# Kernel optimization log

Hardware: AMD Instinct MI355X
Metric: run time of the kernel (lower is better)

The kernel has to match this reference:

```python
import jax, jax.numpy as jnp
import numpy as np

D_MODEL = 1024
NUM_HEADS = 16
D_IN = 1024

def setup_inputs() -> dict:
    key = jax.random.key(0)
    ks = jax.random.split(key, 5)
    scale = 1.0 / np.sqrt(D_IN)
    return {
        "in_features": jax.random.normal(ks[0], (4, 2048, D_IN), dtype=jnp.float32),
        "q_weight": jax.random.normal(ks[1], (D_MODEL, D_IN), dtype=jnp.float32) * scale,
        "k_weight": jax.random.normal(ks[2], (D_MODEL, D_IN), dtype=jnp.float32) * scale,
        "v_weight": jax.random.normal(ks[3], (D_MODEL, D_IN), dtype=jnp.float32) * scale,
        "o_weight": jax.random.normal(ks[4], (D_MODEL, D_MODEL), dtype=jnp.float32) * scale,
    }

def reference(in_features, q_weight, k_weight, v_weight, o_weight):
    batch, seq_len, _ = in_features.shape
    d_head = D_MODEL // NUM_HEADS
    # QKV projections (Linear with no bias: x @ W^T)
    q = jnp.einsum('bsi,di->bsd', in_features, q_weight)
    k = jnp.einsum('bsi,di->bsd', in_features, k_weight)
    v = jnp.einsum('bsi,di->bsd', in_features, v_weight)
    # split heads -> [b, h, s, d_head]
    q = q.reshape(batch, seq_len, NUM_HEADS, d_head).transpose(0, 2, 1, 3)
    k = k.reshape(batch, seq_len, NUM_HEADS, d_head).transpose(0, 2, 1, 3)
    v = v.reshape(batch, seq_len, NUM_HEADS, d_head).transpose(0, 2, 1, 3)
    # scaled dot-product attention (scale by per-head dim, as in SelfAttention)
    scores = jnp.einsum('bhqd,bhkd->bhqk', q, k) / jnp.sqrt(jnp.float32(d_head))
    probs = jax.nn.softmax(scores, axis=-1)
    ctx = jnp.einsum('bhqk,bhkd->bhqd', probs, v)
    # merge heads -> [b, s, d_model]
    ctx = ctx.transpose(0, 2, 1, 3).reshape(batch, seq_len, D_MODEL)
    # output projection
    return jnp.einsum('bsd,md->bsm', ctx, o_weight)
```

## Files before the change

### kernel.cpp

```cpp
#include <hip/hip_runtime.h>

typedef _Float16 half8 __attribute__((ext_vector_type(8)));
typedef _Float16 half4v __attribute__((ext_vector_type(4)));
typedef float f32x4 __attribute__((ext_vector_type(4)));
typedef float f32x16 __attribute__((ext_vector_type(16)));

__device__ __forceinline__ void gload_lds16(const _Float16* g, _Float16* l) {
    __builtin_amdgcn_global_load_lds(
        (const __attribute__((address_space(1))) void*)g,
        (__attribute__((address_space(3))) void*)l,
        16, 0, 0);
}

__global__ void cvt_f32_f16(const float* __restrict__ src, _Float16* __restrict__ dst, int n4) {
    int i = blockIdx.x * blockDim.x + threadIdx.x;
    if (i >= n4) return;
    f32x4 v = ((const f32x4*)src)[i];
    half4v h;
    h[0] = (_Float16)v[0]; h[1] = (_Float16)v[1];
    h[2] = (_Float16)v[2]; h[3] = (_Float16)v[3];
    ((half4v*)dst)[i] = h;
}

__global__ void cvt4_f32_f16(const float* __restrict__ s0, const float* __restrict__ s1,
                             const float* __restrict__ s2, const float* __restrict__ s3,
                             _Float16* __restrict__ dst) {
    int i = blockIdx.x * blockDim.x + threadIdx.x;
    int wsel = blockIdx.y;
    const float* src = (wsel == 0) ? s0 : (wsel == 1) ? s1 : (wsel == 2) ? s2 : s3;
    f32x4 v = ((const f32x4*)src)[i];
    half4v h;
    h[0] = (_Float16)v[0]; h[1] = (_Float16)v[1];
    h[2] = (_Float16)v[2]; h[3] = (_Float16)v[3];
    ((half4v*)(dst + (size_t)wsel * 1048576))[i] = h;
}

template<int MODE>
__global__ void gemm_nt(const _Float16* __restrict__ A,
                        const _Float16* __restrict__ Wbase,
                        void* __restrict__ outbase)
{
    constexpr int K = 1024;
    __shared__ _Float16 As[2][128 * 32];
    __shared__ _Float16 Bs[2][128 * 32];

    const int tid  = threadIdx.x;
    const int lane = tid & 63;
    const int w    = tid >> 6;
    const int wr   = w >> 1, wc = w & 1;
    const int lr   = lane & 15, lg = lane >> 4;
    const int brow = blockIdx.x * 128;
    const int bcol = blockIdx.y * 128;

    const _Float16* Bw = Wbase + (MODE == 0 ? (size_t)blockIdx.z * (1024u * 1024u) : 0);

    const int srow = w * 16 + (lane >> 2);
    const int scol = (lane & 3) * 8;
    const _Float16* Ag = A  + (size_t)(brow + srow) * K + scol;
    const _Float16* Bg = Bw + (size_t)(bcol + srow) * K + scol;

    auto stage = [&](int buf, int kt) {
        const _Float16* a0 = Ag + kt * 32;
        const _Float16* b0 = Bg + kt * 32;
        gload_lds16(a0,           &As[buf][w * 512]);
        gload_lds16(a0 + 64 * K,  &As[buf][w * 512 + 2048]);
        gload_lds16(b0,           &Bs[buf][w * 512]);
        gload_lds16(b0 + 64 * K,  &Bs[buf][w * 512 + 2048]);
    };

    f32x4 acc[4][4] = {};
    stage(0, 0);
    __syncthreads();

    for (int kt = 0; kt < K / 32; ++kt) {
        const int cur = kt & 1;
        if (kt + 1 < K / 32) stage(cur ^ 1, kt + 1);
        half8 af[4], bf[4];
#pragma unroll
        for (int mi = 0; mi < 4; ++mi)
            af[mi] = *(const half8*)&As[cur][(wr * 64 + mi * 16 + lr) * 32 + lg * 8];
#pragma unroll
        for (int ni = 0; ni < 4; ++ni)
            bf[ni] = *(const half8*)&Bs[cur][(wc * 64 + ni * 16 + lr) * 32 + lg * 8];
#pragma unroll
        for (int mi = 0; mi < 4; ++mi)
#pragma unroll
            for (int ni = 0; ni < 4; ++ni)
                acc[mi][ni] = __builtin_amdgcn_mfma_f32_16x16x32_f16(af[mi], bf[ni], acc[mi][ni], 0, 0, 0);
        __syncthreads();
    }

    if (MODE == 0) {
        _Float16* outp = (_Float16*)outbase + (size_t)blockIdx.z * (8192u * 1024u);
        if (blockIdx.z == 2) {
            _Float16* Ts = &As[0][0];
#pragma unroll
            for (int p = 0; p < 2; ++p) {
                if (wc == p) {
#pragma unroll
                    for (int mi = 0; mi < 4; ++mi)
#pragma unroll
                        for (int ni = 0; ni < 4; ++ni) {
                            int drow = ni * 16 + lr;
                            int s0   = wr * 64 + mi * 16 + lg * 4;
                            half4v o;
#pragma unroll
                            for (int r = 0; r < 4; ++r) o[r] = (_Float16)acc[mi][ni][r];
                            int byteoff = drow * 256 + s0 * 2;
                            byteoff ^= (drow & 7) << 4;
                            *(half4v*)((char*)Ts + byteoff) = o;
                        }
                }
                __syncthreads();
                {
                    int row   = tid >> 2;
                    int cbase = (tid & 3) * 4;
                    int gd = bcol + p * 64 + row;
                    int h = gd >> 6, dd = gd & 63;
                    int b = brow >> 11, sseq = brow & 2047;
                    _Float16* gout = outp + (((size_t)b * 16 + h) * 64 + dd) * 2048 + sseq;
#pragma unroll
                    for (int j = 0; j < 4; ++j) {
                        int c  = cbase + j;
                        int lc = c ^ (row & 7);
                        half8 v = *(const half8*)&Ts[row * 128 + lc * 8];
                        *(half8*)&gout[c * 8] = v;
                    }
                }
                __syncthreads();
            }
        } else {
            const float scale = (blockIdx.z == 0) ? 0.18033688f : 1.0f;
#pragma unroll
            for (int mi = 0; mi < 4; ++mi)
#pragma unroll
                for (int ni = 0; ni < 4; ++ni)
#pragma unroll
                    for (int r = 0; r < 4; ++r) {
                        int row = brow + wr * 64 + mi * 16 + lg * 4 + r;
                        int col = bcol + wc * 64 + ni * 16 + lr;
                        int b = row >> 11, s = row & 2047;
                        int h = col >> 6,  d = col & 63;
                        outp[(((size_t)b * 16 + h) * 2048 + s) * 64 + d] =
                            (_Float16)(acc[mi][ni][r] * scale);
                    }
        }
    } else {
        float* outp = (float*)outbase;
#pragma unroll
        for (int mi = 0; mi < 4; ++mi)
#pragma unroll
            for (int ni = 0; ni < 4; ++ni)
#pragma unroll
                for (int r = 0; r < 4; ++r) {
                    int row = brow + wr * 64 + mi * 16 + lg * 4 + r;
                    int col = bcol + wc * 64 + ni * 16 + lr;
                    outp[(size_t)row * 1024 + col] = acc[mi][ni][r];
                }
    }
}

__global__ __launch_bounds__(256, 4)
void attn_kernel(const _Float16* __restrict__ Q,
                 const _Float16* __restrict__ Kx,
                 const _Float16* __restrict__ Vt,
                 _Float16* __restrict__ Ctx)
{
    __shared__ _Float16 Ks[2][64 * 72];
    __shared__ _Float16 Vs[2][64 * 72];

    const int tid = threadIdx.x, lane = tid & 63, w = tid >> 6;
    const int l31 = lane & 31, hi = lane >> 5;
    const int bh = blockIdx.y, qblk = blockIdx.x;

    const _Float16* Qp  = Q  + ((size_t)bh * 2048 + qblk * 128) * 64;
    const _Float16* Kp  = Kx + (size_t)bh * 2048 * 64;
    const _Float16* Vtp = Vt + (size_t)bh * 64 * 2048;

    half8 qf[4];
#pragma unroll
    for (int ks = 0; ks < 4; ++ks)
        qf[ks] = *(const half8*)(Qp + (size_t)(w * 32 + l31) * 64 + ks * 16 + hi * 8);

    half8 ones;
#pragma unroll
    for (int e = 0; e < 8; ++e) ones[e] = (_Float16)1.0f;

    const int srow = tid >> 3;
    const int scol = (tid & 7) * 8;
    const _Float16* Kg0 = Kp  + (size_t)srow * 64   + scol;
    const _Float16* Vg0 = Vtp + (size_t)srow * 2048 + scol;
    const int ldso = srow * 72 + scol;

    f32x16 cacc[2] = {};
    f32x16 lsum = {};
    float m = -1e30f;

    half8 kr0, kr1, vr0, vr1;
    kr0 = *(const half8*)(Kg0);
    kr1 = *(const half8*)(Kg0 + 32 * 64);
    vr0 = *(const half8*)(Vg0);
    vr1 = *(const half8*)(Vg0 + 32 * 2048);
    *(half8*)&Ks[0][ldso]           = kr0;
    *(half8*)&Ks[0][ldso + 32 * 72] = kr1;
    *(half8*)&Vs[0][ldso]           = vr0;
    *(half8*)&Vs[0][ldso + 32 * 72] = vr1;
    __syncthreads();

    for (int t = 0; t < 32; ++t) {
        const int cur = t & 1;
        if (t < 31) {
            kr0 = *(const half8*)(Kg0 + (size_t)(t + 1) * 4096);
            kr1 = *(const half8*)(Kg0 + (size_t)(t + 1) * 4096 + 32 * 64);
        }

        f32x16 sf[2];
        __builtin_amdgcn_s_setprio(1);
#pragma unroll
        for (int kt = 0; kt < 2; ++kt) {
            f32x16 z = {};
#pragma unroll
            for (int ks = 0; ks < 4; ++ks) {
                half8 kf = *(const half8*)&Ks[cur][(kt * 32 + l31) * 72 + ks * 16 + hi * 8];
                z = __builtin_amdgcn_mfma_f32_32x32x16_f16(kf, qf[ks], z, 0, 0, 0);
            }
            sf[kt] = z;
        }
        __builtin_amdgcn_s_setprio(0);

        if (t < 31) {
            *(half8*)&Ks[cur ^ 1][ldso]           = kr0;
            *(half8*)&Ks[cur ^ 1][ldso + 32 * 72] = kr1;
            vr0 = *(const half8*)(Vg0 + (t + 1) * 64);
            vr1 = *(const half8*)(Vg0 + (t + 1) * 64 + 32 * 2048);
        }

        float t8[8];
#pragma unroll
        for (int r = 0; r < 8; ++r)
            t8[r] = fmaxf(fmaxf(sf[0][r], sf[0][r + 8]), fmaxf(sf[1][r], sf[1][r + 8]));
#pragma unroll
        for (int r = 0; r < 4; ++r) t8[r] = fmaxf(t8[r], t8[r + 4]);
        float pmax = fmaxf(fmaxf(t8[0], t8[2]), fmaxf(t8[1], t8[3]));
        pmax = fmaxf(pmax, __shfl_xor(pmax, 32, 64));

        if (!__all(pmax <= m + 8.0f)) {
            float mn = fmaxf(m, pmax);
            float sc = __builtin_amdgcn_exp2f(m - mn);
            cacc[0] = cacc[0] * sc;
            cacc[1] = cacc[1] * sc;
            lsum = lsum * sc;
            m = mn;
        }

#pragma unroll
        for (int kt = 0; kt < 2; ++kt)
#pragma unroll
            for (int r = 0; r < 16; ++r)
                sf[kt][r] = __builtin_amdgcn_exp2f(sf[kt][r] - m);

        unsigned uq[2][4][2];
#pragma unroll
        for (int kt = 0; kt < 2; ++kt)
#pragma unroll
            for (int qd = 0; qd < 4; ++qd)
#pragma unroll
                for (int w2 = 0; w2 < 2; ++w2)
                    uq[kt][qd][w2] = __builtin_bit_cast(unsigned,
                        __builtin_amdgcn_cvt_pkrtz(sf[kt][4 * qd + 2 * w2],
                                                   sf[kt][4 * qd + 2 * w2 + 1]));

        half8 bf[4];
#pragma unroll
        for (int ks = 0; ks < 4; ++ks) {
            const int kt = ks >> 1, k1 = ks & 1;
            union { half8 h; unsigned u[4]; } bu;
#pragma unroll
            for (int w2 = 0; w2 < 2; ++w2) {
                unsigned a = uq[kt][2 * k1][w2];
                unsigned b = uq[kt][2 * k1 + 1][w2];
                unsigned send = hi ? a : b;
                unsigned recv = (unsigned)__shfl_xor((int)send, 32, 64);
                bu.u[w2]     = hi ? recv : a;
                bu.u[2 + w2] = hi ? b : recv;
            }
            bf[ks] = bu.h;
        }

        __builtin_amdgcn_s_setprio(1);
#pragma unroll
        for (int dt = 0; dt < 2; ++dt)
#pragma unroll
            for (int ks = 0; ks < 4; ++ks) {
                half8 vf = *(const half8*)&Vs[cur][(dt * 32 + l31) * 72 + ks * 16 + hi * 8];
                cacc[dt] = __builtin_amdgcn_mfma_f32_32x32x16_f16(vf, bf[ks], cacc[dt], 0, 0, 0);
            }
#pragma unroll
        for (int ks = 0; ks < 4; ++ks)
            lsum = __builtin_amdgcn_mfma_f32_32x32x16_f16(ones, bf[ks], lsum, 0, 0, 0);
        __builtin_amdgcn_s_setprio(0);

        if (t < 31) {
            *(half8*)&Vs[cur ^ 1][ldso]           = vr0;
            *(half8*)&Vs[cur ^ 1][ldso + 32 * 72] = vr1;
        }
        __syncthreads();
    }

    const float inv = 1.0f / lsum[0];
    const int s = qblk * 128 + w * 32 + l31;
    _Float16* Cp = Ctx + ((size_t)(bh >> 4) * 2048 + s) * 1024 + (bh & 15) * 64;
#pragma unroll
    for (int dt = 0; dt < 2; ++dt)
#pragma unroll
        for (int qd = 0; qd < 4; ++qd) {
            half4v o;
#pragma unroll
            for (int j = 0; j < 4; ++j) o[j] = (_Float16)(cacc[dt][4 * qd + j] * inv);
            *(half4v*)&Cp[dt * 32 + qd * 8 + hi * 4] = o;
        }
}

extern "C" void kernel_launch(void* const* d_in, const int* in_sizes, int n_in,
                              void* d_out, int out_size, void* d_ws, size_t ws_size,
                              hipStream_t stream)
{
    const float* X  = (const float*)d_in[0];
    const float* Wq = (const float*)d_in[1];
    const float* Wk = (const float*)d_in[2];
    const float* Wv = (const float*)d_in[3];
    const float* Wo = (const float*)d_in[4];

    if (ws_size < (size_t)(8 + 4 + 24) * 1024 * 1024 * 2) return;
    _Float16* Xh  = (_Float16*)d_ws;
    _Float16* Wh  = Xh + (size_t)8 * 1024 * 1024;
    _Float16* QKV = Wh + (size_t)4 * 1024 * 1024;
    _Float16* Ctx = Xh;

    cvt_f32_f16<<<8192, 256, 0, stream>>>(X, Xh, 2097152);
    cvt4_f32_f16<<<dim3(1024, 4), 256, 0, stream>>>(Wq, Wk, Wv, Wo, Wh);

    gemm_nt<0><<<dim3(64, 8, 3), 256, 0, stream>>>(Xh, Wh, QKV);

    attn_kernel<<<dim3(16, 64), 256, 0, stream>>>(QKV, QKV + 8388608, QKV + 16777216, Ctx);

    gemm_nt<1><<<dim3(64, 8, 1), 256, 0, stream>>>(Ctx, Wh + 3145728, d_out);
}
```

Measured before the change: 220.5 us.

## Software-pipeline QK^T and softmax/PV across half-tiles in attention loop

Splits each 64-key tile into two 32-key halves and restructures the loop so the QK^T MFMAs for one half are issued while the softmax and PV work of the previous half runs. This overlaps matrix-core and VALU/exp work. The row sum is now accumulated with scalar adds plus a final cross-lane shuffle, replacing the ones-vector MFMAs. Two syncs per iteration are now needed, and the online max is updated per half-tile, which adds more rescale checks and raises register pressure.

```diff
diff --git a/kernel.cpp b/kernel.cpp
--- a/kernel.cpp
+++ b/kernel.cpp
@@ -182,10 +182,6 @@
     for (int ks = 0; ks < 4; ++ks)
         qf[ks] = *(const half8*)(Qp + (size_t)(w * 32 + l31) * 64 + ks * 16 + hi * 8);
 
-    half8 ones;
-#pragma unroll
-    for (int e = 0; e < 8; ++e) ones[e] = (_Float16)1.0f;
-
     const int srow = tid >> 3;
     const int scol = (tid & 7) * 8;
     const _Float16* Kg0 = Kp  + (size_t)srow * 64   + scol;
@@ -193,12 +189,82 @@
     const int ldso = srow * 72 + scol;
 
     f32x16 cacc[2] = {};
-    f32x16 lsum = {};
-    float m = -1e30f;
+    float m = -1e30f, l = 0.f;
+
+    auto qkt = [&](int kbuf, int kt) -> f32x16 {
+        f32x16 z = {};
+#pragma unroll
+        for (int ks = 0; ks < 4; ++ks) {
+            half8 kf = *(const half8*)&Ks[kbuf][(kt * 32 + l31) * 72 + ks * 16 + hi * 8];
+            z = __builtin_amdgcn_mfma_f32_32x32x16_f16(kf, qf[ks], z, 0, 0, 0);
+        }
+        return z;
+    };
+
+    auto finish = [&](f32x16& sf, int vbuf, int kt) {
+        float t4[4];
+#pragma unroll
+        for (int r = 0; r < 4; ++r)
+            t4[r] = fmaxf(fmaxf(sf[r], sf[r + 4]), fmaxf(sf[r + 8], sf[r + 12]));
+        float pmax = fmaxf(fmaxf(t4[0], t4[1]), fmaxf(t4[2], t4[3]));
+        pmax = fmaxf(pmax, __shfl_xor(pmax, 32, 64));
+
+        if (!__all(pmax <= m + 8.0f)) {
+            float mn = fmaxf(m, pmax);
+            float sc = __builtin_amdgcn_exp2f(m - mn);
+            cacc[0] = cacc[0] * sc;
+            cacc[1] = cacc[1] * sc;
+            l *= sc;
+            m = mn;
+        }
+
+        float rsum = 0.f;
+#pragma unroll
+        for (int r = 0; r < 16; ++r) {
+            float p = __builtin_amdgcn_exp2f(sf[r] - m);
+            sf[r] = p;
+            rsum += p;
+        }
+        l += rsum;
+
+        unsigned uq[4][2];
+#pragma unroll
+        for (int qd = 0; qd < 4; ++qd)
+#pragma unroll
+            for (int w2 = 0; w2 < 2; ++w2)
+                uq[qd][w2] = __builtin_bit_cast(unsigned,
+                    __builtin_amdgcn_cvt_pkrtz(sf[4 * qd + 2 * w2], sf[4 * qd + 2 * w2 + 1]));
+
+        half8 bf[2];
+#pragma unroll
+        for (int k1 = 0; k1 < 2; ++k1) {
+            union { half8 h; unsigned u[4]; } bu;
+#pragma unroll
+            for (int w2 = 0; w2 < 2; ++w2) {
+                unsigned a = uq[2 * k1][w2];
+                unsigned b = uq[2 * k1 + 1][w2];
+                unsigned send = hi ? a : b;
+                unsigned recv = (unsigned)__shfl_xor((int)send, 32, 64);
+                bu.u[w2]     = hi ? recv : a;
+                bu.u[2 + w2] = hi ? b : recv;
+            }
+            bf[k1] = bu.h;
+        }
+
+        __builtin_amdgcn_s_setprio(1);
+#pragma unroll
+        for (int dt = 0; dt < 2; ++dt)
+#pragma unroll
+            for (int k1 = 0; k1 < 2; ++k1) {
+                half8 vf = *(const half8*)&Vs[vbuf][(dt * 32 + l31) * 72 + kt * 32 + k1 * 16 + hi * 8];
+                cacc[dt] = __builtin_amdgcn_mfma_f32_32x32x16_f16(vf, bf[k1], cacc[dt], 0, 0, 0);
+            }
+        __builtin_amdgcn_s_setprio(0);
+    };
 
     half8 kr0, kr1, vr0, vr1;
     kr0 = *(const half8*)(Kg0);
-    kr1 = *(const half8*)(Kg0 + 32 * 64);
+    kr1 = *(const half8*)(Kg0 + 2048);
     vr0 = *(const half8*)(Vg0);
     vr1 = *(const half8*)(Vg0 + 32 * 2048);
     *(half8*)&Ks[0][ldso]           = kr0;
@@ -207,107 +273,45 @@
     *(half8*)&Vs[0][ldso + 32 * 72] = vr1;
     __syncthreads();
 
-    for (int t = 0; t < 32; ++t) {
+    kr0 = *(const half8*)(Kg0 + 4096);
+    kr1 = *(const half8*)(Kg0 + 4096 + 2048);
+    vr0 = *(const half8*)(Vg0 + 64);
+    vr1 = *(const half8*)(Vg0 + 64 + 32 * 2048);
+    f32x16 sf0, sf1;
+    sf0 = qkt(0, 0);
+    finish(sf0, 0, 0);
+    sf1 = qkt(0, 1);
+    __syncthreads();
+    *(half8*)&Ks[1][ldso]           = kr0;
+    *(half8*)&Ks[1][ldso + 32 * 72] = kr1;
+    *(half8*)&Vs[1][ldso]           = vr0;
+    *(half8*)&Vs[1][ldso + 32 * 72] = vr1;
+    __syncthreads();
+
+    for (int t = 1; t < 32; ++t) {
         const int cur = t & 1;
         if (t < 31) {
             kr0 = *(const half8*)(Kg0 + (size_t)(t + 1) * 4096);
-            kr1 = *(const half8*)(Kg0 + (size_t)(t + 1) * 4096 + 32 * 64);
-        }
-
-        f32x16 sf[2];
-        __builtin_amdgcn_s_setprio(1);
-#pragma unroll
-        for (int kt = 0; kt < 2; ++kt) {
-            f32x16 z = {};
-#pragma unroll
-            for (int ks = 0; ks < 4; ++ks) {
-                half8 kf = *(const half8*)&Ks[cur][(kt * 32 + l31) * 72 + ks * 16 + hi * 8];
-                z = __builtin_amdgcn_mfma_f32_32x32x16_f16(kf, qf[ks], z, 0, 0, 0);
-            }
-            sf[kt] = z;
-        }
-        __builtin_amdgcn_s_setprio(0);
-
+            kr1 = *(const half8*)(Kg0 + (size_t)(t + 1) * 4096 + 2048);
+            vr0 = *(const half8*)(Vg0 + (t + 1) * 64);
+            vr1 = *(const half8*)(Vg0 + (t + 1) * 64 + 32 * 2048);
+        }
+        sf0 = qkt(cur, 0);
+        finish(sf1, cur ^ 1, 1);
+        sf1 = qkt(cur, 1);
+        finish(sf0, cur, 0);
+        __syncthreads();
         if (t < 31) {
             *(half8*)&Ks[cur ^ 1][ldso]           = kr0;
             *(half8*)&Ks[cur ^ 1][ldso + 32 * 72] = kr1;
-            vr0 = *(const half8*)(Vg0 + (t + 1) * 64);
-            vr1 = *(const half8*)(Vg0 + (t + 1) * 64 + 32 * 2048);
-        }
-
-        float t8[8];
-#pragma unroll
-        for (int r = 0; r < 8; ++r)
-            t8[r] = fmaxf(fmaxf(sf[0][r], sf[0][r + 8]), fmaxf(sf[1][r], sf[1][r + 8]));
-#pragma unroll
-        for (int r = 0; r < 4; ++r) t8[r] = fmaxf(t8[r], t8[r + 4]);
-        float pmax = fmaxf(fmaxf(t8[0], t8[2]), fmaxf(t8[1], t8[3]));
-        pmax = fmaxf(pmax, __shfl_xor(pmax, 32, 64));
-
-        if (!__all(pmax <= m + 8.0f)) {
-            float mn = fmaxf(m, pmax);
-            float sc = __builtin_amdgcn_exp2f(m - mn);
-            cacc[0] = cacc[0] * sc;
-            cacc[1] = cacc[1] * sc;
-            lsum = lsum * sc;
-            m = mn;
-        }
-
-#pragma unroll
-        for (int kt = 0; kt < 2; ++kt)
-#pragma unroll
-            for (int r = 0; r < 16; ++r)
-                sf[kt][r] = __builtin_amdgcn_exp2f(sf[kt][r] - m);
-
-        unsigned uq[2][4][2];
-#pragma unroll
-        for (int kt = 0; kt < 2; ++kt)
-#pragma unroll
-            for (int qd = 0; qd < 4; ++qd)
-#pragma unroll
-                for (int w2 = 0; w2 < 2; ++w2)
-                    uq[kt][qd][w2] = __builtin_bit_cast(unsigned,
-                        __builtin_amdgcn_cvt_pkrtz(sf[kt][4 * qd + 2 * w2],
-                                                   sf[kt][4 * qd + 2 * w2 + 1]));
-
-        half8 bf[4];
-#pragma unroll
-        for (int ks = 0; ks < 4; ++ks) {
-            const int kt = ks >> 1, k1 = ks & 1;
-            union { half8 h; unsigned u[4]; } bu;
-#pragma unroll
-            for (int w2 = 0; w2 < 2; ++w2) {
-                unsigned a = uq[kt][2 * k1][w2];
-                unsigned b = uq[kt][2 * k1 + 1][w2];
-                unsigned send = hi ? a : b;
-                unsigned recv = (unsigned)__shfl_xor((int)send, 32, 64);
-                bu.u[w2]     = hi ? recv : a;
-                bu.u[2 + w2] = hi ? b : recv;
-            }
-            bf[ks] = bu.h;
-        }
-
-        __builtin_amdgcn_s_setprio(1);
-#pragma unroll
-        for (int dt = 0; dt < 2; ++dt)
-#pragma unroll
-            for (int ks = 0; ks < 4; ++ks) {
-                half8 vf = *(const half8*)&Vs[cur][(dt * 32 + l31) * 72 + ks * 16 + hi * 8];
-                cacc[dt] = __builtin_amdgcn_mfma_f32_32x32x16_f16(vf, bf[ks], cacc[dt], 0, 0, 0);
-            }
-#pragma unroll
-        for (int ks = 0; ks < 4; ++ks)
-            lsum = __builtin_amdgcn_mfma_f32_32x32x16_f16(ones, bf[ks], lsum, 0, 0, 0);
-        __builtin_amdgcn_s_setprio(0);
-
-        if (t < 31) {
             *(half8*)&Vs[cur ^ 1][ldso]           = vr0;
             *(half8*)&Vs[cur ^ 1][ldso + 32 * 72] = vr1;
         }
         __syncthreads();
     }
-
-    const float inv = 1.0f / lsum[0];
+    finish(sf1, 1, 1);
+
+    const float inv = 1.0f / (l + __shfl_xor(l, 32, 64));
     const int s = qblk * 128 + w * 32 + l31;
     _Float16* Cp = Ctx + ((size_t)(bh >> 4) * 2048 + s) * 1024 + (bh & 15) * 64;
 #pragma unroll
```

New measurement: 219.4 us. About the same (-0.5%).
